# Kernel tuning notes

Hardware: AMD Instinct MI355X
Metric: run time of the kernel (lower is better)

## Reference

```python
import jax, jax.numpy as jnp
import numpy as np

E, H, NH = 512, 2048, 8
HD = E // NH
EPS = 1e-5


def setup_inputs() -> dict:
    key = jax.random.key(0)
    ks = jax.random.split(key, 13)
    s = lambda k, shape, fan_in: jax.random.normal(k, shape, dtype=jnp.float32) * (1.0 / np.sqrt(fan_in))
    return {
        "x": jax.random.normal(ks[0], (1, 4096, E), dtype=jnp.float32),
        "ln_g": jnp.ones((E,), jnp.float32),
        "ln_b": jnp.zeros((E,), jnp.float32),
        "qkv_w": s(ks[1], (3 * E, E), E),
        "qkv_b": jnp.zeros((3 * E,), jnp.float32),
        "proj_w": s(ks[2], (E, E), E),
        "proj_b": jnp.zeros((E,), jnp.float32),
        "fc1_w": s(ks[3], (H, E), E),
        "fc1_b": jnp.zeros((H,), jnp.float32),
        "fc2_w": s(ks[4], (H, H), H),
        "fc2_b": jnp.zeros((H,), jnp.float32),
        "fc3_w": s(ks[5], (E, H), H),
        "fc3_b": jnp.zeros((E,), jnp.float32),
    }


def _layernorm(x, g, b):
    mu = jnp.mean(x, axis=-1, keepdims=True)
    var = jnp.mean(jnp.square(x - mu), axis=-1, keepdims=True)
    return (x - mu) * jax.lax.rsqrt(var + EPS) * g + b


def _attention(h, qkv_w, qkv_b, proj_w, proj_b):
    B, N, _ = h.shape
    qkv = h @ qkv_w.T + qkv_b                      # [B, N, 3E]
    qkv = qkv.reshape(B, N, 3, NH, HD).transpose(2, 0, 3, 1, 4)  # [3, B, NH, N, HD]
    q, k, v = qkv[0], qkv[1], qkv[2]
    scale = HD ** -0.5
    scores = jnp.einsum("bhqd,bhkd->bhqk", q, k) * scale  # full N x N matrix (faithful)
    probs = jax.nn.softmax(scores, axis=-1)
    out = jnp.einsum("bhqk,bhkd->bhqd", probs, v)  # [B, NH, N, HD]
    out = out.transpose(0, 2, 1, 3).reshape(B, N, E)
    return out @ proj_w.T + proj_b


def _mlp(h, fc1_w, fc1_b, fc2_w, fc2_b, fc3_w, fc3_b):
    h = jax.nn.relu(h @ fc1_w.T + fc1_b)
    h = jax.nn.relu(h @ fc2_w.T + fc2_b)
    return h @ fc3_w.T + fc3_b


def reference(x, ln_g, ln_b, qkv_w, qkv_b, proj_w, proj_b,
              fc1_w, fc1_b, fc2_w, fc2_b, fc3_w, fc3_b):
    # Pre-norm block; note the SAME LayerNorm params are used for both sublayers
    x = x + _attention(_layernorm(x, ln_g, ln_b), qkv_w, qkv_b, proj_w, proj_b)
    x = x + _mlp(_layernorm(x, ln_g, ln_b), fc1_w, fc1_b, fc2_w, fc2_b, fc3_w, fc3_b)
    return x
```

## Files before the change

### kernel.cpp

```cpp
#include <hip/hip_runtime.h>
#include <cstdint>
#include <cstddef>

typedef _Float16 f16;
typedef f16 f16x8 __attribute__((ext_vector_type(8)));
typedef f16 f16x4 __attribute__((ext_vector_type(4)));
typedef float f32x4 __attribute__((ext_vector_type(4)));

#define SLEN 4096
#define EDIM 512
#define TEDIM 1536
#define HDIM 2048
#define NHEAD 8
#define HD 64
#define NSPLIT 4

#define LDS_ASYNC16(gp, lp)                                                      \
  __builtin_amdgcn_global_load_lds(                                              \
      (__attribute__((address_space(1))) void*)(void*)(gp),                      \
      (__attribute__((address_space(3))) void*)(void*)(lp), 16, 0, 0)


struct CvtArgs {
  const float* src[5];
  f16* dst[5];
};
__global__ __launch_bounds__(256) void cvt_all(CvtArgs a) {
  int b = blockIdx.x;
  int seg, off;
  if (b < 384)       { seg = 0; off = b; }
  else if (b < 512)  { seg = 1; off = b - 384; }
  else if (b < 1024) { seg = 2; off = b - 512; }
  else if (b < 3072) { seg = 3; off = b - 1024; }
  else               { seg = 4; off = b - 3072; }
  int i = (off * 256 + threadIdx.x) * 8;
  const float* src = a.src[seg];
  f16* dst = a.dst[seg];
  float4 x = *(const float4*)(src + i);
  float4 y = *(const float4*)(src + i + 4);
  f16x8 o;
  o[0] = (f16)x.x; o[1] = (f16)x.y; o[2] = (f16)x.z; o[3] = (f16)x.w;
  o[4] = (f16)y.x; o[5] = (f16)y.y; o[6] = (f16)y.z; o[7] = (f16)y.w;
  *(f16x8*)(dst + i) = o;
}

__global__ __launch_bounds__(256) void ln_kernel(const float* __restrict__ src,
                                                 const float* __restrict__ g,
                                                 const float* __restrict__ b,
                                                 f16* __restrict__ out) {
  int wave = threadIdx.x >> 6, lane = threadIdx.x & 63;
  int row = blockIdx.x * 4 + wave;
  const float* p = src + (size_t)row * EDIM + lane * 8;
  float v[8];
  float4 a = *(const float4*)p;
  float4 c = *(const float4*)(p + 4);
  v[0] = a.x; v[1] = a.y; v[2] = a.z; v[3] = a.w;
  v[4] = c.x; v[5] = c.y; v[6] = c.z; v[7] = c.w;
  float s = 0.f, s2 = 0.f;
#pragma unroll
  for (int j = 0; j < 8; ++j) { s += v[j]; s2 += v[j] * v[j]; }
#pragma unroll
  for (int m = 1; m < 64; m <<= 1) {
    s += __shfl_xor(s, m, 64);
    s2 += __shfl_xor(s2, m, 64);
  }
  float mu = s * (1.0f / 512.0f);
  float var = s2 * (1.0f / 512.0f) - mu * mu;
  float rs = rsqrtf(var + 1e-5f);
  float4 gg = *(const float4*)(g + lane * 8);
  float4 gh = *(const float4*)(g + lane * 8 + 4);
  float4 bb = *(const float4*)(b + lane * 8);
  float4 bh = *(const float4*)(b + lane * 8 + 4);
  float ga[8] = {gg.x, gg.y, gg.z, gg.w, gh.x, gh.y, gh.z, gh.w};
  float ba[8] = {bb.x, bb.y, bb.z, bb.w, bh.x, bh.y, bh.z, bh.w};
  f16x8 o;
#pragma unroll
  for (int j = 0; j < 8; ++j) o[j] = (f16)((v[j] - mu) * rs * ga[j] + ba[j]);
  *(f16x8*)(out + (size_t)row * EDIM + lane * 8) = o;
}

template <int RELU, int RES, int OUTF32, int BN>
__global__ __launch_bounds__(256) void gemm_bt(const f16* __restrict__ A,
                                               const f16* __restrict__ W,
                                               const float* __restrict__ bias,
                                               const float* __restrict__ res,
                                               void* __restrict__ out,
                                               int M, int Nn, int K) {
  constexpr int MF = (BN == 128) ? 4 : 2;
  __shared__ f16 lA[128 * 64];
  __shared__ f16 lB[BN * 64];
  const int t = threadIdx.x;
  const int wave = t >> 6, lane = t & 63;
  const int wm = (BN == 128) ? (wave >> 1) : wave;
  const int wn = (BN == 128) ? (wave & 1) : 0;
  const int quad = lane >> 4, l15 = lane & 15;
  const int m0 = blockIdx.y * 128, n0 = blockIdx.x * BN;

  f32x4 acc[MF][4] = {};

  const int srow = t >> 3;
  const int scol = (((t & 7) ^ (srow & 7))) * 8;
  const f16* gA = A + (size_t)(m0 + srow) * K + scol;
  const f16* gB = W + (size_t)(n0 + srow) * K + scol;
  const int sw = (l15 & 7);

  for (int k0 = 0; k0 < K; k0 += 64) {
    __syncthreads();
#pragma unroll
    for (int is = 0; is < 4; ++is)
      LDS_ASYNC16(gA + (size_t)(is * 32) * K + k0, lA + is * 2048 + wave * 512);
#pragma unroll
    for (int is = 0; is < BN / 32; ++is)
      LDS_ASYNC16(gB + (size_t)(is * 32) * K + k0, lB + is * 2048 + wave * 512);
    __syncthreads();
#pragma unroll
    for (int ks = 0; ks < 2; ++ks) {
      f16x8 af[MF], bfv[4];
#pragma unroll
      for (int mf = 0; mf < MF; ++mf)
        af[mf] = *(const f16x8*)(lA + (wm * (MF * 16) + mf * 16 + l15) * 64 +
                                 ((ks * 4 + quad) ^ sw) * 8);
#pragma unroll
      for (int nf = 0; nf < 4; ++nf)
        bfv[nf] = *(const f16x8*)(lB + (wn * 64 + nf * 16 + l15) * 64 +
                                  ((ks * 4 + quad) ^ sw) * 8);
#pragma unroll
      for (int mf = 0; mf < MF; ++mf)
#pragma unroll
        for (int nf = 0; nf < 4; ++nf)
          acc[mf][nf] =
              __builtin_amdgcn_mfma_f32_16x16x32_f16(af[mf], bfv[nf], acc[mf][nf], 0, 0, 0);
    }
  }

  const int mbase = m0 + wm * (MF * 16);
  const int nbase = n0 + wn * 64;
  float bv[4];
#pragma unroll
  for (int nf = 0; nf < 4; ++nf) bv[nf] = bias[nbase + nf * 16 + l15];
#pragma unroll
  for (int mf = 0; mf < MF; ++mf) {
#pragma unroll
    for (int r = 0; r < 4; ++r) {
      size_t m = mbase + mf * 16 + quad * 4 + r;
#pragma unroll
      for (int nf = 0; nf < 4; ++nf) {
        int n = nbase + nf * 16 + l15;
        float v = acc[mf][nf][r] + bv[nf];
        if (RELU) v = v > 0.f ? v : 0.f;
        if (RES) v += res[m * Nn + n];
        if (OUTF32)
          ((float*)out)[m * Nn + n] = v;
        else
          ((f16*)out)[m * Nn + n] = (f16)v;
      }
    }
  }
}

__global__ __launch_bounds__(256) void build_vt(const f16* __restrict__ qkv,
                                                f16* __restrict__ vt) {
  __shared__ f16 tile[64 * 72];
  const int h = blockIdx.x >> 6, nt = blockIdx.x & 63;
  const int t = threadIdx.x;
  const int n0 = nt * 64;
#pragma unroll
  for (int is = 0; is < 2; ++is) {
    int e = is * 2048 + t * 8;
    int nl = e >> 6, d = e & 63;
    f16x8 v = *(const f16x8*)(qkv + (size_t)(n0 + nl) * TEDIM + 1024 + h * 64 + d);
    *(f16x8*)(tile + nl * 72 + d) = v;
  }
  __syncthreads();
  const int d = t >> 2, nc = (t & 3) * 16;
  union { f16 e[16]; f16x8 v[2]; } buf;
#pragma unroll
  for (int j = 0; j < 16; ++j) buf.e[j] = tile[(nc + j) * 72 + d];
  f16* dst = vt + (size_t)h * 64 * SLEN + (size_t)d * SLEN + n0 + nc;
  *(f16x8*)dst = buf.v[0];
  *(f16x8*)(dst + 8) = buf.v[1];
}

__global__ __launch_bounds__(256) void attn_kernel(const f16* __restrict__ qkv,
                                                   const f16* __restrict__ vt,
                                                   f16* __restrict__ Opart,
                                                   float* __restrict__ Lpart) {
  __shared__ f16 lK[64 * 64];
  __shared__ f16 lV[64 * 64];
  const int t = threadIdx.x, wave = t >> 6, lane = t & 63;
  const int quad = lane >> 4, l15 = lane & 15;
  const int split = blockIdx.x & 3;
  const int qb = (blockIdx.x >> 2) & 31;
  const int h = blockIdx.x >> 7;
  const int q0 = qb * 128 + wave * 32;
  const int kv0 = split * (SLEN / NSPLIT);
  const int sw = (l15 & 7);

  f16x8 qf[2][2];
#pragma unroll
  for (int mf = 0; mf < 2; ++mf)
#pragma unroll
    for (int ks = 0; ks < 2; ++ks) {
      f16x8 v = *(const f16x8*)(qkv + (size_t)(q0 + mf * 16 + l15) * TEDIM + h * 64 +
                                ks * 32 + quad * 8);
#pragma unroll
      for (int j = 0; j < 8; ++j) v[j] = v[j] * (f16)0.125f;
      qf[mf][ks] = v;
    }

  f32x4 o[2][4] = {};
  float lsum[2] = {0.f, 0.f};

  const int srow = t >> 3;
  const int scol = ((t & 7) ^ (srow & 7)) * 8;
  const f16* gK = qkv + (size_t)(kv0 + srow) * TEDIM + 512 + h * 64 + scol;
  const f16* gV = vt + (size_t)h * 64 * SLEN + (size_t)srow * SLEN + kv0 + scol;

  for (int kt = 0; kt < (SLEN / NSPLIT) / 64; ++kt) {
    __syncthreads();
#pragma unroll
    for (int is = 0; is < 2; ++is) {
      LDS_ASYNC16(gK + (size_t)(kt * 64 + is * 32) * TEDIM, lK + is * 2048 + wave * 512);
      LDS_ASYNC16(gV + (size_t)(is * 32) * SLEN + kt * 64, lV + is * 2048 + wave * 512);
    }
    __syncthreads();

    f32x4 st[4][2] = {};
#pragma unroll
    for (int ks = 0; ks < 2; ++ks) {
      f16x8 kfr[4];
#pragma unroll
      for (int cf = 0; cf < 4; ++cf)
        kfr[cf] = *(const f16x8*)(lK + (cf * 16 + l15) * 64 + ((ks * 4 + quad) ^ sw) * 8);
#pragma unroll
      for (int cf = 0; cf < 4; ++cf)
#pragma unroll
        for (int mf = 0; mf < 2; ++mf)
          st[cf][mf] =
              __builtin_amdgcn_mfma_f32_16x16x32_f16(kfr[cf], qf[mf][ks], st[cf][mf], 0, 0, 0);
    }

    f16x4 pf[4][2];
#pragma unroll
    for (int cf = 0; cf < 4; ++cf)
#pragma unroll
      for (int mf = 0; mf < 2; ++mf)
#pragma unroll
        for (int r = 0; r < 4; ++r) {
          float p = __expf(st[cf][mf][r]);
          lsum[mf] += p;
          pf[cf][mf][r] = (f16)p;
        }

#pragma unroll
    for (int cf = 0; cf < 4; ++cf) {
      f16x4 vfr[4];
#pragma unroll
      for (int nf = 0; nf < 4; ++nf)
        vfr[nf] = *(const f16x4*)(lV + (nf * 16 + l15) * 64 +
                                  (((cf * 2 + (quad >> 1)) ^ sw) * 8) + (quad & 1) * 4);
#pragma unroll
      for (int mf = 0; mf < 2; ++mf)
#pragma unroll
        for (int nf = 0; nf < 4; ++nf)
          o[mf][nf] = __builtin_amdgcn_mfma_f32_16x16x16f16(pf[cf][mf], vfr[nf], o[mf][nf], 0, 0, 0);
    }
  }

#pragma unroll
  for (int mf = 0; mf < 2; ++mf) {
    float v = lsum[mf];
    v += __shfl_xor(v, 16, 64);
    v += __shfl_xor(v, 32, 64);
    if (quad == 0) Lpart[(size_t)(split * NHEAD + h) * SLEN + q0 + mf * 16 + l15] = v;
  }
#pragma unroll
  for (int mf = 0; mf < 2; ++mf)
#pragma unroll
    for (int r = 0; r < 4; ++r) {
      int row = q0 + mf * 16 + quad * 4 + r;
      f16* dst = Opart + ((size_t)split * SLEN + row) * EDIM + h * 64;
#pragma unroll
      for (int nf = 0; nf < 4; ++nf) dst[nf * 16 + l15] = (f16)o[mf][nf][r];
    }
}

__global__ __launch_bounds__(256) void attn_combine(const f16* __restrict__ Opart,
                                                    const float* __restrict__ Lpart,
                                                    f16* __restrict__ attn) {
  int idx = (blockIdx.x * 256 + threadIdx.x) * 8;
  int row = idx >> 9;
  int col = idx & 511;
  int h = col >> 6;
  float l = 0.f;
#pragma unroll
  for (int s = 0; s < NSPLIT; ++s) l += Lpart[((size_t)s * NHEAD + h) * SLEN + row];
  float inv = 1.0f / l;
  float acc[8] = {};
#pragma unroll
  for (int s = 0; s < NSPLIT; ++s) {
    f16x8 a = *(const f16x8*)(Opart + ((size_t)s * SLEN + row) * EDIM + col);
#pragma unroll
    for (int j = 0; j < 8; ++j) acc[j] += (float)a[j];
  }
  f16x8 o;
#pragma unroll
  for (int j = 0; j < 8; ++j) o[j] = (f16)(acc[j] * inv);
  *(f16x8*)(attn + (size_t)row * EDIM + col) = o;
}

extern "C" void kernel_launch(void* const* d_in, const int* in_sizes, int n_in,
                              void* d_out, int out_size, void* d_ws, size_t ws_size,
                              hipStream_t stream) {
  const float* x      = (const float*)d_in[0];
  const float* ln_g   = (const float*)d_in[1];
  const float* ln_b   = (const float*)d_in[2];
  const float* qkv_w  = (const float*)d_in[3];
  const float* qkv_b  = (const float*)d_in[4];
  const float* proj_w = (const float*)d_in[5];
  const float* proj_b = (const float*)d_in[6];
  const float* fc1_w  = (const float*)d_in[7];
  const float* fc1_b  = (const float*)d_in[8];
  const float* fc2_w  = (const float*)d_in[9];
  const float* fc2_b  = (const float*)d_in[10];
  const float* fc3_w  = (const float*)d_in[11];
  const float* fc3_b  = (const float*)d_in[12];
  float* out = (float*)d_out;

  char* w = (char*)d_ws;
  f16* wq = (f16*)(w);
  f16* wp = (f16*)(w + (2ull << 20));
  f16* w1 = (f16*)(w + (3ull << 20));
  f16* w2 = (f16*)(w + (5ull << 20));
  f16* w3 = (f16*)(w + (13ull << 20));
  f16* ws_qkv   = (f16*)(w + (15ull << 20));
  f16* ws_vt    = (f16*)(w + (27ull << 20));
  f16* ws_opart = (f16*)(w + (31ull << 20));
  float* ws_lp  = (float*)(w + (47ull << 20));
  f16* ws_attn  = (f16*)(w + (48ull << 20));
  f16* ws_h1    = (f16*)(w + (31ull << 20));
  float* ws_x1  = (float*)(w + (31ull << 20));
  f16* ws_h2    = (f16*)(w + (39ull << 20));
  f16* ws_m1    = (f16*)(w + (15ull << 20));
  f16* ws_m2    = (f16*)(w + (39ull << 20));

  CvtArgs ca;
  ca.src[0] = qkv_w; ca.src[1] = proj_w; ca.src[2] = fc1_w; ca.src[3] = fc2_w; ca.src[4] = fc3_w;
  ca.dst[0] = wq;    ca.dst[1] = wp;     ca.dst[2] = w1;    ca.dst[3] = w2;    ca.dst[4] = w3;
  cvt_all<<<3584, 256, 0, stream>>>(ca);

  ln_kernel<<<SLEN / 4, 256, 0, stream>>>(x, ln_g, ln_b, ws_h1);
  gemm_bt<0, 0, 0, 128><<<dim3(TEDIM / 128, SLEN / 128), 256, 0, stream>>>(
      ws_h1, wq, qkv_b, nullptr, ws_qkv, SLEN, TEDIM, EDIM);
  build_vt<<<NHEAD * (SLEN / 64), 256, 0, stream>>>(ws_qkv, ws_vt);
  attn_kernel<<<NHEAD * (SLEN / 128) * NSPLIT, 256, 0, stream>>>(ws_qkv, ws_vt, ws_opart, ws_lp);
  attn_combine<<<(SLEN * EDIM) / 2048, 256, 0, stream>>>(ws_opart, ws_lp, ws_attn);
  gemm_bt<0, 1, 1, 64><<<dim3(EDIM / 64, SLEN / 128), 256, 0, stream>>>(
      ws_attn, wp, proj_b, x, ws_x1, SLEN, EDIM, EDIM);
  ln_kernel<<<SLEN / 4, 256, 0, stream>>>(ws_x1, ln_g, ln_b, ws_h2);
  gemm_bt<1, 0, 0, 128><<<dim3(HDIM / 128, SLEN / 128), 256, 0, stream>>>(
      ws_h2, w1, fc1_b, nullptr, ws_m1, SLEN, HDIM, EDIM);
  gemm_bt<1, 0, 0, 128><<<dim3(HDIM / 128, SLEN / 128), 256, 0, stream>>>(
      ws_m1, w2, fc2_b, nullptr, ws_m2, SLEN, HDIM, HDIM);
  gemm_bt<0, 1, 1, 64><<<dim3(EDIM / 64, SLEN / 128), 256, 0, stream>>>(
      ws_m2, w3, fc3_b, ws_x1, out, SLEN, EDIM, HDIM);
}
```

Before: 288.8 us.

## Fuse weight cast with first LayerNorm, tune GEMM BK, MFMA-based softmax row sums

New measurement: 284.4 us. No clear change (-1.5%).

```diff
diff --git a/kernel.cpp b/kernel.cpp
--- a/kernel.cpp
+++ b/kernel.cpp
@@ -5,6 +5,7 @@
 typedef _Float16 f16;
 typedef f16 f16x8 __attribute__((ext_vector_type(8)));
 typedef f16 f16x4 __attribute__((ext_vector_type(4)));
+typedef __fp16 h16x2 __attribute__((ext_vector_type(2)));
 typedef float f32x4 __attribute__((ext_vector_type(4)));
 
 #define SLEN 4096
@@ -25,23 +26,58 @@
   const float* src[5];
   f16* dst[5];
 };
-__global__ __launch_bounds__(256) void cvt_all(CvtArgs a) {
+__global__ __launch_bounds__(256) void prep_kernel(CvtArgs a, const float* __restrict__ x,
+                                                   const float* __restrict__ g,
+                                                   const float* __restrict__ bb_,
+                                                   f16* __restrict__ h1) {
   int b = blockIdx.x;
-  int seg, off;
-  if (b < 384)       { seg = 0; off = b; }
-  else if (b < 512)  { seg = 1; off = b - 384; }
-  else if (b < 1024) { seg = 2; off = b - 512; }
-  else if (b < 3072) { seg = 3; off = b - 1024; }
-  else               { seg = 4; off = b - 3072; }
-  int i = (off * 256 + threadIdx.x) * 8;
-  const float* src = a.src[seg];
-  f16* dst = a.dst[seg];
-  float4 x = *(const float4*)(src + i);
-  float4 y = *(const float4*)(src + i + 4);
+  if (b < 3584) {
+    int seg, off;
+    if (b < 384)       { seg = 0; off = b; }
+    else if (b < 512)  { seg = 1; off = b - 384; }
+    else if (b < 1024) { seg = 2; off = b - 512; }
+    else if (b < 3072) { seg = 3; off = b - 1024; }
+    else               { seg = 4; off = b - 3072; }
+    int i = (off * 256 + threadIdx.x) * 8;
+    const float* src = a.src[seg];
+    f16* dst = a.dst[seg];
+    float4 p = *(const float4*)(src + i);
+    float4 q = *(const float4*)(src + i + 4);
+    f16x8 o;
+    o[0] = (f16)p.x; o[1] = (f16)p.y; o[2] = (f16)p.z; o[3] = (f16)p.w;
+    o[4] = (f16)q.x; o[5] = (f16)q.y; o[6] = (f16)q.z; o[7] = (f16)q.w;
+    *(f16x8*)(dst + i) = o;
+    return;
+  }
+  int wave = threadIdx.x >> 6, lane = threadIdx.x & 63;
+  int row = (b - 3584) * 4 + wave;
+  const float* p = x + (size_t)row * EDIM + lane * 8;
+  float v[8];
+  float4 aa = *(const float4*)p;
+  float4 cc = *(const float4*)(p + 4);
+  v[0] = aa.x; v[1] = aa.y; v[2] = aa.z; v[3] = aa.w;
+  v[4] = cc.x; v[5] = cc.y; v[6] = cc.z; v[7] = cc.w;
+  float s = 0.f, s2 = 0.f;
+#pragma unroll
+  for (int j = 0; j < 8; ++j) { s += v[j]; s2 += v[j] * v[j]; }
+#pragma unroll
+  for (int m = 1; m < 64; m <<= 1) {
+    s += __shfl_xor(s, m, 64);
+    s2 += __shfl_xor(s2, m, 64);
+  }
+  float mu = s * (1.0f / 512.0f);
+  float var = s2 * (1.0f / 512.0f) - mu * mu;
+  float rs = rsqrtf(var + 1e-5f);
+  float4 gg = *(const float4*)(g + lane * 8);
+  float4 gh = *(const float4*)(g + lane * 8 + 4);
+  float4 bl = *(const float4*)(bb_ + lane * 8);
+  float4 bh = *(const float4*)(bb_ + lane * 8 + 4);
+  float ga[8] = {gg.x, gg.y, gg.z, gg.w, gh.x, gh.y, gh.z, gh.w};
+  float ba[8] = {bl.x, bl.y, bl.z, bl.w, bh.x, bh.y, bh.z, bh.w};
   f16x8 o;
-  o[0] = (f16)x.x; o[1] = (f16)x.y; o[2] = (f16)x.z; o[3] = (f16)x.w;
-  o[4] = (f16)y.x; o[5] = (f16)y.y; o[6] = (f16)y.z; o[7] = (f16)y.w;
-  *(f16x8*)(dst + i) = o;
+#pragma unroll
+  for (int j = 0; j < 8; ++j) o[j] = (f16)((v[j] - mu) * rs * ga[j] + ba[j]);
+  *(f16x8*)(h1 + (size_t)row * EDIM + lane * 8) = o;
 }
 
 __global__ __launch_bounds__(256) void ln_kernel(const float* __restrict__ src,
@@ -79,7 +115,7 @@
   *(f16x8*)(out + (size_t)row * EDIM + lane * 8) = o;
 }
 
-template <int RELU, int RES, int OUTF32, int BN>
+template <int RELU, int RES, int OUTF32, int BN, int BK>
 __global__ __launch_bounds__(256) void gemm_bt(const f16* __restrict__ A,
                                                const f16* __restrict__ W,
                                                const float* __restrict__ bias,
@@ -87,8 +123,12 @@
                                                void* __restrict__ out,
                                                int M, int Nn, int K) {
   constexpr int MF = (BN == 128) ? 4 : 2;
-  __shared__ f16 lA[128 * 64];
-  __shared__ f16 lB[BN * 64];
+  constexpr int GPR = BK / 8;
+  constexpr int RPA = 256 / GPR;
+  constexpr int NA_A = 128 / RPA;
+  constexpr int NA_B = BN / RPA;
+  __shared__ f16 lA[128 * BK];
+  __shared__ f16 lB[BN * BK];
   const int t = threadIdx.x;
   const int wave = t >> 6, lane = t & 63;
   const int wm = (BN == 128) ? (wave >> 1) : wave;
@@ -98,31 +138,31 @@
 
   f32x4 acc[MF][4] = {};
 
-  const int srow = t >> 3;
-  const int scol = (((t & 7) ^ (srow & 7))) * 8;
+  const int srow = t / GPR;
+  const int scol = ((t % GPR) ^ (srow & 7)) * 8;
   const f16* gA = A + (size_t)(m0 + srow) * K + scol;
   const f16* gB = W + (size_t)(n0 + srow) * K + scol;
   const int sw = (l15 & 7);
 
-  for (int k0 = 0; k0 < K; k0 += 64) {
+  for (int k0 = 0; k0 < K; k0 += BK) {
     __syncthreads();
 #pragma unroll
-    for (int is = 0; is < 4; ++is)
-      LDS_ASYNC16(gA + (size_t)(is * 32) * K + k0, lA + is * 2048 + wave * 512);
-#pragma unroll
-    for (int is = 0; is < BN / 32; ++is)
-      LDS_ASYNC16(gB + (size_t)(is * 32) * K + k0, lB + is * 2048 + wave * 512);
+    for (int is = 0; is < NA_A; ++is)
+      LDS_ASYNC16(gA + (size_t)(is * RPA) * K + k0, lA + is * 2048 + wave * 512);
+#pragma unroll
+    for (int is = 0; is < NA_B; ++is)
+      LDS_ASYNC16(gB + (size_t)(is * RPA) * K + k0, lB + is * 2048 + wave * 512);
     __syncthreads();
 #pragma unroll
-    for (int ks = 0; ks < 2; ++ks) {
+    for (int ks = 0; ks < BK / 32; ++ks) {
       f16x8 af[MF], bfv[4];
 #pragma unroll
       for (int mf = 0; mf < MF; ++mf)
-        af[mf] = *(const f16x8*)(lA + (wm * (MF * 16) + mf * 16 + l15) * 64 +
+        af[mf] = *(const f16x8*)(lA + (wm * (MF * 16) + mf * 16 + l15) * BK +
                                  ((ks * 4 + quad) ^ sw) * 8);
 #pragma unroll
       for (int nf = 0; nf < 4; ++nf)
-        bfv[nf] = *(const f16x8*)(lB + (wn * 64 + nf * 16 + l15) * 64 +
+        bfv[nf] = *(const f16x8*)(lB + (wn * 64 + nf * 16 + l15) * BK +
                                   ((ks * 4 + quad) ^ sw) * 8);
 #pragma unroll
       for (int mf = 0; mf < MF; ++mf)
@@ -209,7 +249,10 @@
     }
 
   f32x4 o[2][4] = {};
-  float lsum[2] = {0.f, 0.f};
+  f32x4 o5[2] = {};
+  f16x4 ones;
+#pragma unroll
+  for (int j = 0; j < 4; ++j) ones[j] = (l15 == 0) ? (f16)1.0f : (f16)0.0f;
 
   const int srow = t >> 3;
   const int scol = ((t & 7) ^ (srow & 7)) * 8;
@@ -246,10 +289,12 @@
 #pragma unroll
       for (int mf = 0; mf < 2; ++mf)
 #pragma unroll
-        for (int r = 0; r < 4; ++r) {
-          float p = __expf(st[cf][mf][r]);
-          lsum[mf] += p;
-          pf[cf][mf][r] = (f16)p;
+        for (int rp = 0; rp < 2; ++rp) {
+          float p0 = __expf(st[cf][mf][2 * rp]);
+          float p1 = __expf(st[cf][mf][2 * rp + 1]);
+          h16x2 pk = __builtin_amdgcn_cvt_pkrtz(p0, p1);
+          pf[cf][mf][2 * rp] = (f16)pk[0];
+          pf[cf][mf][2 * rp + 1] = (f16)pk[1];
         }
 
 #pragma unroll
@@ -260,19 +305,21 @@
         vfr[nf] = *(const f16x4*)(lV + (nf * 16 + l15) * 64 +
                                   (((cf * 2 + (quad >> 1)) ^ sw) * 8) + (quad & 1) * 4);
 #pragma unroll
-      for (int mf = 0; mf < 2; ++mf)
+      for (int mf = 0; mf < 2; ++mf) {
 #pragma unroll
         for (int nf = 0; nf < 4; ++nf)
           o[mf][nf] = __builtin_amdgcn_mfma_f32_16x16x16f16(pf[cf][mf], vfr[nf], o[mf][nf], 0, 0, 0);
-    }
-  }
-
-#pragma unroll
-  for (int mf = 0; mf < 2; ++mf) {
-    float v = lsum[mf];
-    v += __shfl_xor(v, 16, 64);
-    v += __shfl_xor(v, 32, 64);
-    if (quad == 0) Lpart[(size_t)(split * NHEAD + h) * SLEN + q0 + mf * 16 + l15] = v;
+        o5[mf] = __builtin_amdgcn_mfma_f32_16x16x16f16(pf[cf][mf], ones, o5[mf], 0, 0, 0);
+      }
+    }
+  }
+
+  if (l15 == 0) {
+#pragma unroll
+    for (int mf = 0; mf < 2; ++mf)
+#pragma unroll
+      for (int r = 0; r < 4; ++r)
+        Lpart[(size_t)(split * NHEAD + h) * SLEN + q0 + mf * 16 + quad * 4 + r] = o5[mf][r];
   }
 #pragma unroll
   for (int mf = 0; mf < 2; ++mf)
@@ -347,21 +394,20 @@
   CvtArgs ca;
   ca.src[0] = qkv_w; ca.src[1] = proj_w; ca.src[2] = fc1_w; ca.src[3] = fc2_w; ca.src[4] = fc3_w;
   ca.dst[0] = wq;    ca.dst[1] = wp;     ca.dst[2] = w1;    ca.dst[3] = w2;    ca.dst[4] = w3;
-  cvt_all<<<3584, 256, 0, stream>>>(ca);
-
-  ln_kernel<<<SLEN / 4, 256, 0, stream>>>(x, ln_g, ln_b, ws_h1);
-  gemm_bt<0, 0, 0, 128><<<dim3(TEDIM / 128, SLEN / 128), 256, 0, stream>>>(
+  prep_kernel<<<3584 + SLEN / 4, 256, 0, stream>>>(ca, x, ln_g, ln_b, ws_h1);
+
+  gemm_bt<0, 0, 0, 128, 128><<<dim3(TEDIM / 128, SLEN / 128), 256, 0, stream>>>(
       ws_h1, wq, qkv_b, nullptr, ws_qkv, SLEN, TEDIM, EDIM);
   build_vt<<<NHEAD * (SLEN / 64), 256, 0, stream>>>(ws_qkv, ws_vt);
   attn_kernel<<<NHEAD * (SLEN / 128) * NSPLIT, 256, 0, stream>>>(ws_qkv, ws_vt, ws_opart, ws_lp);
   attn_combine<<<(SLEN * EDIM) / 2048, 256, 0, stream>>>(ws_opart, ws_lp, ws_attn);
-  gemm_bt<0, 1, 1, 64><<<dim3(EDIM / 64, SLEN / 128), 256, 0, stream>>>(
+  gemm_bt<0, 1, 1, 64, 128><<<dim3(EDIM / 64, SLEN / 128), 256, 0, stream>>>(
       ws_attn, wp, proj_b, x, ws_x1, SLEN, EDIM, EDIM);
   ln_kernel<<<SLEN / 4, 256, 0, stream>>>(ws_x1, ln_g, ln_b, ws_h2);
-  gemm_bt<1, 0, 0, 128><<<dim3(HDIM / 128, SLEN / 128), 256, 0, stream>>>(
+  gemm_bt<1, 0, 0, 128, 128><<<dim3(HDIM / 128, SLEN / 128), 256, 0, stream>>>(
       ws_h2, w1, fc1_b, nullptr, ws_m1, SLEN, HDIM, EDIM);
-  gemm_bt<1, 0, 0, 128><<<dim3(HDIM / 128, SLEN / 128), 256, 0, stream>>>(
+  gemm_bt<1, 0, 0, 128, 64><<<dim3(HDIM / 128, SLEN / 128), 256, 0, stream>>>(
       ws_m1, w2, fc2_b, nullptr, ws_m2, SLEN, HDIM, HDIM);
-  gemm_bt<0, 1, 1, 64><<<dim3(EDIM / 64, SLEN / 128), 256, 0, stream>>>(
+  gemm_bt<0, 1, 1, 64, 64><<<dim3(EDIM / 64, SLEN / 128), 256, 0, stream>>>(
       ws_m2, w3, fc3_b, ws_x1, out, SLEN, EDIM, HDIM);
 }
```
